# Optimization experiments

Measured on AMD Instinct MI355X. Metric: run time of the kernel, lower is better.

Reference implementation:

```python
import jax, jax.numpy as jnp
import numpy as np

CONSTRAINT_WEIGHT = 0.5
FOCAL_GAMMA = 2.0
EPS = 1e-8

B, G, C = 65536, 9, 9
BLK = 3  # int(sqrt(G))


def setup_inputs() -> dict:
    key = jax.random.key(0)
    k1, k2, k3 = jax.random.split(key, 3)
    logits = jax.random.normal(k1, (B, G, G, C), dtype=jnp.float32)
    targets = jax.random.randint(k2, (B, G, G), 0, 10, dtype=jnp.int64)
    puzzles = jax.random.randint(k3, (B, G, G), 0, 10, dtype=jnp.int64)
    return {"logits": logits, "targets": targets, "puzzles": puzzles}


def _sudoku_loss(logits, targets, puzzles):
    b, g, _, c = logits.shape
    mask = (puzzles == 0).astype(logits.dtype)            # [B,G,G]
    tgt = jnp.clip(targets - 1, 0, c - 1)                 # [B,G,G]

    log_probs = jax.nn.log_softmax(logits, axis=-1)       # [B,G,G,C]
    probs = jnp.exp(log_probs)

    # --- focal CE over masked (empty) cells ---
    lp_t = jnp.take_along_axis(log_probs, tgt[..., None], axis=-1)[..., 0]  # [B,G,G]
    pt = jnp.exp(lp_t)
    ce = -lp_t
    focal = (1.0 - pt) ** FOCAL_GAMMA * ce
    msum = mask.sum()
    ce_loss = (focal * mask).sum() / (msum + EPS)

    # --- constraint loss ---
    masked_probs = probs * mask[..., None]                # [B,G,G,C]
    row_sums = masked_probs.sum(axis=2)                   # [B,G,C]
    row_loss = jnp.mean((row_sums - 1.0) ** 2)
    col_sums = masked_probs.sum(axis=1)                   # [B,G,C]
    col_loss = jnp.mean((col_sums - 1.0) ** 2)
    # boxes: [B, br, r, bc, c_in, C] -> sum over the 3x3 cells of each box
    box = masked_probs.reshape(b, BLK, BLK, BLK, BLK, c)
    box_sums = box.transpose(0, 1, 3, 2, 4, 5).reshape(b, BLK * BLK, BLK * BLK, c).sum(axis=2)
    box_loss = jnp.mean((box_sums - 1.0) ** 2)

    entropy = -(probs * log_probs).sum(axis=-1)           # [B,G,G]
    entropy_loss = 0.1 * ((entropy * mask).sum() / (msum + EPS))

    top2, _ = jax.lax.top_k(probs, 2)                     # [B,G,G,2]
    gap = top2[..., 0] - top2[..., 1]
    uniqueness_loss = 0.1 * jnp.mean(jax.nn.relu(1.0 - gap))

    constraint_loss = (row_loss + col_loss + box_loss + entropy_loss + uniqueness_loss) * 0.2
    return ce_loss + CONSTRAINT_WEIGHT * constraint_loss


def reference(logits, targets, puzzles):
    return _sudoku_loss(logits, targets, puzzles)
```

## Files before the change

kernel.cpp:

```cpp
#include <hip/hip_runtime.h>

#define THREADS 256
#define PB 3
#define ROWW 84

typedef float f4 __attribute__((ext_vector_type(4)));
typedef f4 f4u __attribute__((aligned(4)));

__global__ __launch_bounds__(THREADS) void sudoku_main(
    const float* __restrict__ logits,
    const int*   __restrict__ targets,
    const int*   __restrict__ puzzles,
    float* __restrict__ acc,
    int B)
{
  __shared__ float probT[PB * 9 * ROWW];
  __shared__ float sred[4][5];

  const int tid  = threadIdx.x;
  const int lp   = tid / 81;
  const int cell = tid % 81;
  const bool workerA = tid < 243;
  const int cp   = tid / 9;
  const int numGroups = (B + PB - 1) / PB;

  float a_focal = 0.f, a_ent = 0.f, a_msk = 0.f, a_uniq = 0.f, a_sq = 0.f;

  for (int g = blockIdx.x; g < numGroups; g += gridDim.x) {
    const int grp = min(PB, B - g * PB);

    if (workerA && lp < grp) {
      const size_t cidx = (size_t)g * (PB * 81) + tid;
      const float* Lp = logits + cidx * 9;
      f4 v0 = *(const f4u*)(Lp);
      f4 v1 = *(const f4u*)(Lp + 4);
      float l8 = Lp[8];
      int tg = targets[cidx] - 1;
      int pz = puzzles[cidx];
      tg = tg < 0 ? 0 : (tg > 8 ? 8 : tg);

      float l[9];
      l[0]=v0[0]; l[1]=v0[1]; l[2]=v0[2]; l[3]=v0[3];
      l[4]=v1[0]; l[5]=v1[1]; l[6]=v1[2]; l[7]=v1[3]; l[8]=l8;

      float t1 = l[0], t2 = -3.0e38f;
#pragma unroll
      for (int i = 1; i < 9; ++i) {
        float hi = fmaxf(t1, l[i]);
        float lo = fminf(t1, l[i]);
        t1 = hi;
        t2 = fmaxf(t2, lo);
      }

      float e[9], s = 0.f, lsum = 0.f, ltg = l[0];
#pragma unroll
      for (int i = 0; i < 9; ++i) {
        float x  = l[i] - t1;
        float ei = __expf(x);
        e[i] = ei;
        s += ei;
        lsum = fmaf(ei, x, lsum);
        if (i > 0) ltg = (tg == i) ? l[i] : ltg;
      }
      float inv_s = __builtin_amdgcn_rcpf(s);
      float logs  = __logf(s);

      float lpt   = (ltg - t1) - logs;
      float pt    = __expf(lpt);
      float om    = 1.f - pt;
      float focal = om * om * (-lpt);

      float ent = logs - lsum * inv_s;
      float gap = (1.f - __expf(t2 - t1)) * inv_s;
      float uq  = fmaxf(0.f, 1.f - gap);

      float mk = (pz == 0) ? 1.f : 0.f;
      a_focal += focal * mk;
      a_ent   += ent * mk;
      a_msk   += mk;
      a_uniq  += uq;

      float pm = inv_s * mk;
#pragma unroll
      for (int i = 0; i < 9; ++i)
        probT[(lp * 9 + i) * ROWW + cell] = e[i] * pm;
    }
    __syncthreads();

    if (tid < 27 && cp < grp) {
      const float* base = &probT[tid * ROWW];
      float rs[9], cs[9], bs[9];
#pragma unroll
      for (int u = 0; u < 9; ++u) { rs[u] = 0.f; cs[u] = 0.f; bs[u] = 0.f; }
#pragma unroll
      for (int q = 0; q < 20; ++q) {
        f4 v = *(const f4*)(base + q * 4);
#pragma unroll
        for (int j = 0; j < 4; ++j) {
          const int k = q * 4 + j;
          float x = v[j];
          rs[k / 9] += x;
          cs[k % 9] += x;
          bs[(k / 27) * 3 + (k % 9) / 3] += x;
        }
      }
      {
        float x = base[80];
        rs[8] += x; cs[8] += x; bs[8] += x;
      }
#pragma unroll
      for (int u = 0; u < 9; ++u) {
        float dr = rs[u] - 1.f, dc = cs[u] - 1.f, db = bs[u] - 1.f;
        a_sq = fmaf(dr, dr, a_sq);
        a_sq = fmaf(dc, dc, a_sq);
        a_sq = fmaf(db, db, a_sq);
      }
    }
    __syncthreads();
  }

#pragma unroll
  for (int off = 32; off > 0; off >>= 1) {
    a_focal += __shfl_down(a_focal, off);
    a_ent   += __shfl_down(a_ent,   off);
    a_msk   += __shfl_down(a_msk,   off);
    a_uniq  += __shfl_down(a_uniq,  off);
    a_sq    += __shfl_down(a_sq,    off);
  }
  const int wave = tid >> 6;
  if ((tid & 63) == 0) {
    sred[wave][0] = a_focal; sred[wave][1] = a_ent; sred[wave][2] = a_msk;
    sred[wave][3] = a_uniq;  sred[wave][4] = a_sq;
  }
  __syncthreads();
  if (tid < 5) {
    float v = sred[0][tid] + sred[1][tid] + sred[2][tid] + sred[3][tid];
    atomicAdd(&acc[tid], v);
  }
}

__global__ void sudoku_finalize(const float* __restrict__ acc,
                                float* __restrict__ out, float invBG)
{
  float focal = acc[0], ent = acc[1], msum = acc[2], uniq = acc[3], sq = acc[4];
  float inv_m = 1.f / (msum + 1e-8f);
  float ce    = focal * inv_m;
  float entl  = 0.1f * ent * inv_m;
  float uql   = 0.1f * uniq * invBG;
  float rcb   = sq * invBG;
  float constraint = (rcb + entl + uql) * 0.2f;
  out[0] = ce + 0.5f * constraint;
}

extern "C" void kernel_launch(void* const* d_in, const int* in_sizes, int n_in,
                              void* d_out, int out_size, void* d_ws, size_t ws_size,
                              hipStream_t stream)
{
  (void)n_in; (void)out_size; (void)ws_size;
  const float* logits  = (const float*)d_in[0];
  const int*   targets = (const int*)d_in[1];
  const int*   puzzles = (const int*)d_in[2];
  float* out = (float*)d_out;
  float* acc = (float*)d_ws;

  const int B = in_sizes[0] / 729;
  const int numGroups = (B + PB - 1) / PB;

  hipMemsetAsync(acc, 0, 5 * sizeof(float), stream);

  int grid = numGroups < 2048 ? numGroups : 2048;
  sudoku_main<<<grid, THREADS, 0, stream>>>(logits, targets, puzzles, acc, B);

  const float invBG = 1.f / ((float)B * 81.f);
  sudoku_finalize<<<1, 1, 0, stream>>>(acc, out, invBG);
}
```

Measured before the change: 68.77 us.

## Double-buffer shared probs, prefetch next group, spread constraint sums across waves

```diff
diff --git a/kernel.cpp b/kernel.cpp
--- a/kernel.cpp
+++ b/kernel.cpp
@@ -2,10 +2,10 @@
 
 #define THREADS 256
 #define PB 3
-#define ROWW 84
+#define COLW 84
 
 typedef float f4 __attribute__((ext_vector_type(4)));
-typedef f4 f4u __attribute__((aligned(4)));
+typedef f4 f4a4 __attribute__((aligned(4)));
 
 __global__ __launch_bounds__(THREADS) void sudoku_main(
     const float* __restrict__ logits,
@@ -14,34 +14,43 @@
     float* __restrict__ acc,
     int B)
 {
-  __shared__ float probT[PB * 9 * ROWW];
+  __shared__ float probT[2][PB * 9 * COLW];
   __shared__ float sred[4][5];
 
   const int tid  = threadIdx.x;
   const int lp   = tid / 81;
   const int cell = tid % 81;
   const bool workerA = tid < 243;
-  const int cp   = tid / 9;
+  const int cpad = 28 * (cell / 27) + (cell % 27);
+  const int B81  = B * 81;
   const int numGroups = (B + PB - 1) / PB;
+
+  const int cw   = tid >> 6;
+  const int l27  = tid & 63;
+  const bool workerC = (l27 < 27) && (cw < 3);
+  const int ccls = l27 / 3;
+  const int ck   = l27 % 3;
 
   float a_focal = 0.f, a_ent = 0.f, a_msk = 0.f, a_uniq = 0.f, a_sq = 0.f;
 
-  for (int g = blockIdx.x; g < numGroups; g += gridDim.x) {
-    const int grp = min(PB, B - g * PB);
+  int g0 = blockIdx.x;
+  bool vA = workerA && (g0 < numGroups) && (g0 * 243 + tid < B81);
+  f4 c0{}, c1{}; float c8 = 0.f; int ctg = 0, cpz = 0;
+  if (vA) {
+    const float* Lp = logits + (size_t)(g0 * 243 + tid) * 9;
+    c0 = *(const f4a4*)Lp; c1 = *(const f4a4*)(Lp + 4); c8 = Lp[8];
+    ctg = targets[g0 * 243 + tid]; cpz = puzzles[g0 * 243 + tid];
+  }
 
-    if (workerA && lp < grp) {
-      const size_t cidx = (size_t)g * (PB * 81) + tid;
-      const float* Lp = logits + cidx * 9;
-      f4 v0 = *(const f4u*)(Lp);
-      f4 v1 = *(const f4u*)(Lp + 4);
-      float l8 = Lp[8];
-      int tg = targets[cidx] - 1;
-      int pz = puzzles[cidx];
-      tg = tg < 0 ? 0 : (tg > 8 ? 8 : tg);
+  int it = 0;
+  for (int g = blockIdx.x; g < numGroups; g += gridDim.x, ++it) {
+    float* PT = probT[it & 1];
 
+    if (vA) {
       float l[9];
-      l[0]=v0[0]; l[1]=v0[1]; l[2]=v0[2]; l[3]=v0[3];
-      l[4]=v1[0]; l[5]=v1[1]; l[6]=v1[2]; l[7]=v1[3]; l[8]=l8;
+      l[0]=c0[0]; l[1]=c0[1]; l[2]=c0[2]; l[3]=c0[3];
+      l[4]=c1[0]; l[5]=c1[1]; l[6]=c1[2]; l[7]=c1[3]; l[8]=c8;
+      int tg = ctg - 1; tg = tg < 0 ? 0 : (tg > 8 ? 8 : tg);
 
       float t1 = l[0], t2 = -3.0e38f;
 #pragma unroll
@@ -51,7 +60,6 @@
         t1 = hi;
         t2 = fmaxf(t2, lo);
       }
-
       float e[9], s = 0.f, lsum = 0.f, ltg = l[0];
 #pragma unroll
       for (int i = 0; i < 9; ++i) {
@@ -64,59 +72,70 @@
       }
       float inv_s = __builtin_amdgcn_rcpf(s);
       float logs  = __logf(s);
-
       float lpt   = (ltg - t1) - logs;
       float pt    = __expf(lpt);
       float om    = 1.f - pt;
       float focal = om * om * (-lpt);
-
-      float ent = logs - lsum * inv_s;
-      float gap = (1.f - __expf(t2 - t1)) * inv_s;
-      float uq  = fmaxf(0.f, 1.f - gap);
-
-      float mk = (pz == 0) ? 1.f : 0.f;
+      float ent   = logs - lsum * inv_s;
+      float gap   = (1.f - __expf(t2 - t1)) * inv_s;
+      float uq    = fmaxf(0.f, 1.f - gap);
+      float mk    = (cpz == 0) ? 1.f : 0.f;
       a_focal += focal * mk;
       a_ent   += ent * mk;
       a_msk   += mk;
       a_uniq  += uq;
-
       float pm = inv_s * mk;
 #pragma unroll
       for (int i = 0; i < 9; ++i)
-        probT[(lp * 9 + i) * ROWW + cell] = e[i] * pm;
+        PT[(lp * 9 + i) * COLW + cpad] = e[i] * pm;
     }
+
+    const int gn = g + (int)gridDim.x;
+    const bool vAn = workerA && (gn < numGroups) && (gn * 243 + tid < B81);
+    f4 n0{}, n1{}; float n8 = 0.f; int ntg = 0, npz = 0;
+    if (vAn) {
+      const float* Lp = logits + (size_t)(gn * 243 + tid) * 9;
+      n0 = *(const f4a4*)Lp; n1 = *(const f4a4*)(Lp + 4); n8 = Lp[8];
+      ntg = targets[gn * 243 + tid]; npz = puzzles[gn * 243 + tid];
+    }
+
     __syncthreads();
 
-    if (tid < 27 && cp < grp) {
-      const float* base = &probT[tid * ROWW];
-      float rs[9], cs[9], bs[9];
+    if (workerC && (g * PB + cw) < B) {
+      const float* base = PT + (cw * 9 + ccls) * COLW + 28 * ck;
+      float vv[28];
+      ((f4*)vv)[0] = *(const f4*)(base);
+      ((f4*)vv)[1] = *(const f4*)(base + 4);
+      ((f4*)vv)[2] = *(const f4*)(base + 8);
+      ((f4*)vv)[3] = *(const f4*)(base + 12);
+      ((f4*)vv)[4] = *(const f4*)(base + 16);
+      ((f4*)vv)[5] = *(const f4*)(base + 20);
+      ((f4*)vv)[6] = *(const f4*)(base + 24);
+      float rs[3] = {0.f,0.f,0.f}, bs[3] = {0.f,0.f,0.f};
+      float cs[9] = {0.f,0.f,0.f,0.f,0.f,0.f,0.f,0.f,0.f};
 #pragma unroll
-      for (int u = 0; u < 9; ++u) { rs[u] = 0.f; cs[u] = 0.f; bs[u] = 0.f; }
-#pragma unroll
-      for (int q = 0; q < 20; ++q) {
-        f4 v = *(const f4*)(base + q * 4);
-#pragma unroll
-        for (int j = 0; j < 4; ++j) {
-          const int k = q * 4 + j;
-          float x = v[j];
-          rs[k / 9] += x;
-          cs[k % 9] += x;
-          bs[(k / 27) * 3 + (k % 9) / 3] += x;
-        }
-      }
-      {
-        float x = base[80];
-        rs[8] += x; cs[8] += x; bs[8] += x;
+      for (int j = 0; j < 27; ++j) {
+        float v = vv[j];
+        rs[j / 9]       += v;
+        cs[j % 9]       += v;
+        bs[(j % 9) / 3] += v;
       }
 #pragma unroll
-      for (int u = 0; u < 9; ++u) {
-        float dr = rs[u] - 1.f, dc = cs[u] - 1.f, db = bs[u] - 1.f;
-        a_sq = fmaf(dr, dr, a_sq);
-        a_sq = fmaf(dc, dc, a_sq);
-        a_sq = fmaf(db, db, a_sq);
+      for (int r = 0; r < 3; ++r) {
+        float d = rs[r] - 1.f; a_sq = fmaf(d, d, a_sq);
+        d = bs[r] - 1.f;       a_sq = fmaf(d, d, a_sq);
       }
+      float csq = 0.f;
+#pragma unroll
+      for (int c9 = 0; c9 < 9; ++c9) {
+        float t = cs[c9] + __shfl_down(cs[c9], 1) + __shfl_down(cs[c9], 2);
+        float d = t - 1.f;
+        csq = fmaf(d, d, csq);
+      }
+      if (ck == 0) a_sq += csq;
     }
-    __syncthreads();
+
+    vA = vAn; c0 = n0; c1 = n1; c8 = n8; ctg = ntg; cpz = npz;
   }
 
 #pragma unroll
```

Result: faster. 61.04 us (-11.2%).
